# Optimization experiments

Hardware: AMD Instinct MI355X
Metric: run time of the kernel (lower is better)

Reference implementation:

```python
import jax, jax.numpy as jnp
import numpy as np

INFLUENCE_RADIUS = 8  # VectorizedTrajectoryComputer default


def compute_trajectories(emb):
    # emb: [B, S, D] -> [B, S, D]
    B, S, D = emb.shape
    diffs = emb[:, 1:] - emb[:, :-1]                      # [B, S-1, D]
    mag = jnp.linalg.norm(diffs, axis=-1, keepdims=True)  # [B, S-1, 1]
    ntraj = diffs / jnp.maximum(mag, 1e-8)                # normalized trajectories
    mw = jnp.tanh(mag[..., 0])                            # magnitude weights [B, S-1]
    pos = jnp.arange(S)[:, None]                          # [S, 1]
    j = jnp.arange(S - 1)[None, :]                        # [1, S-1]
    ws = jnp.maximum(0, pos - INFLUENCE_RADIUS)           # window start per pos
    mask = (j >= ws) & (j < pos)                          # window_end = pos (pos <= S-1)
    wsz = jnp.maximum(pos - ws, 1)                        # window size (>=1 to avoid /0)
    recency = jnp.where(mask, (j - ws + 1) / wsz, 0.0).astype(emb.dtype)  # [S, S-1]
    cw = mw[:, None, :] * recency[None]                   # combined weights [B, S, S-1]
    nw = cw / jnp.maximum(cw.sum(-1, keepdims=True), 1e-8)
    return jnp.einsum('bpj,bjd->bpd', nw, ntraj)          # [B, S, D]


def setup_inputs() -> dict:
    key = jax.random.key(0)
    ks = jax.random.split(key, 6)
    B, S, D = 2, 2048, 1024
    H, K, hd = 16, 16, 64
    return {
        'x': jax.random.normal(ks[0], (B, S, D), dtype=jnp.float32),
        'qkv_w': jax.random.normal(ks[1], (3 * D, D), dtype=jnp.float32) * 0.02,
        'out_w': jax.random.normal(ks[2], (D, D), dtype=jnp.float32) * 0.02,
        'splat_centers': jax.random.normal(ks[3], (H, K, hd), dtype=jnp.float32) * 0.02,
        'splat_log_scales': jnp.zeros((H, K), dtype=jnp.float32),
        'splat_amplitudes': jnp.ones((H, K), dtype=jnp.float32),
    }


def reference(x, qkv_w, out_w, splat_centers, splat_log_scales, splat_amplitudes):
    B, S, D = x.shape
    H, K, hd = splat_centers.shape
    # trajectories (computed when trajectories=None in forward)
    traj = compute_trajectories(x)
    # qkv projection (no bias)
    qkv = x @ qkv_w.T                                      # [B, S, 3D]
    q, k, v = jnp.split(qkv, 3, axis=-1)
    def heads(t):
        return t.reshape(B, S, H, hd).transpose(0, 2, 1, 3)  # [B, H, S, hd]
    q, k, v = heads(q), heads(k), heads(v)
    # squared distances to splat centers: [B, H, S, K]
    cn = jnp.sum(splat_centers ** 2, axis=-1)              # [H, K]
    def dists_sq(t):
        tn = jnp.sum(t ** 2, axis=-1, keepdims=True)       # [B, H, S, 1]
        cross = jnp.einsum('bhsd,hkd->bhsk', t, splat_centers)
        return tn - 2.0 * cross + cn[None, :, None, :]
    scales_sq = jnp.exp(splat_log_scales)[None, :, None, :] ** 2  # [1, H, 1, K]
    amp = jax.nn.sigmoid(splat_amplitudes)[None, :, None, :]
    q_weights = jnp.exp(-0.5 * dists_sq(q) / scales_sq) * amp     # [B, H, S, K]
    k_weights = jnp.exp(-0.5 * dists_sq(k) / scales_sq) * amp
    attn = jnp.einsum('bhis,bhjs->bhij', q_weights, k_weights)    # [B, H, S, S]
    attn = jax.nn.softmax(attn, axis=-1)
    out = jnp.einsum('bhij,bhjd->bhid', attn, v)                  # [B, H, S, hd]
    out = out.transpose(0, 2, 1, 3).reshape(B, S, D) @ out_w.T    # [B, S, D]
    return out, traj
```

## Files before the change

kernel.cpp:

```cpp
#include <hip/hip_runtime.h>
#include <math.h>

#define SEQ 2048
#define DIM 1024
#define NB  2
#define NH  16

typedef __attribute__((ext_vector_type(8))) short short8;
typedef __attribute__((ext_vector_type(4))) float floatx4;
typedef __attribute__((ext_vector_type(16))) float floatx16;

__device__ __forceinline__ ushort f2bf(float f) {
    unsigned u = __float_as_uint(f);
    return (ushort)((u + 0x7FFFu + ((u >> 16) & 1u)) >> 16);
}
__device__ __forceinline__ float bf2f(ushort h) {
    return __uint_as_float(((unsigned)h) << 16);
}
__device__ __forceinline__ void gload16(const void* g, char* lds_base) {
    __builtin_amdgcn_global_load_lds(
        (const __attribute__((address_space(1))) void*)g,
        (__attribute__((address_space(3))) void*)lds_base, 16, 0, 0);
}
__device__ __forceinline__ unsigned cvtpk(float a, float b) {
    unsigned r;
    asm("v_cvt_pk_bf16_f32 %0, %1, %2" : "=v"(r) : "v"(a), "v"(b));
    return r;
}
__device__ __forceinline__ void plswap(unsigned &a, unsigned &b) {
    asm("v_permlane32_swap_b32 %0, %1" : "+v"(a), "+v"(b));
}

__global__ __launch_bounds__(256) void front_kernel(
    const float* __restrict__ x, const float* __restrict__ qkv_w,
    ushort* __restrict__ xh, ushort* __restrict__ xl,
    ushort* __restrict__ wh, ushort* __restrict__ wlv,
    float* __restrict__ sbuf, float* __restrict__ invbuf)
{
    const int blk = blockIdx.x;
    if (blk < 4096) {
        int i = blk * 1024 + threadIdx.x * 4;
        float4 v = *(const float4*)(x + i);
        ushort4 h, l;
        h.x = f2bf(v.x); l.x = f2bf(v.x - bf2f(h.x));
        h.y = f2bf(v.y); l.y = f2bf(v.y - bf2f(h.y));
        h.z = f2bf(v.z); l.z = f2bf(v.z - bf2f(h.z));
        h.w = f2bf(v.w); l.w = f2bf(v.w - bf2f(h.w));
        *(ushort4*)(xh + i) = h;
        *(ushort4*)(xl + i) = l;
    } else if (blk < 6144) {
        int i = (blk - 4096) * 1024 + threadIdx.x * 4;
        float4 v = *(const float4*)(qkv_w + i);
        ushort4 o;
        o.x = f2bf(v.x); o.y = f2bf(v.y); o.z = f2bf(v.z); o.w = f2bf(v.w);
        *(ushort4*)(wh + i) = o;
    } else if (blk < 7168) {
        int i = (blk - 6144) * 1024 + threadIdx.x * 4;
        float4 v = *(const float4*)(qkv_w + 2097152 + i);
        ushort4 h, l;
        h.x = f2bf(v.x); l.x = f2bf(v.x - bf2f(h.x));
        h.y = f2bf(v.y); l.y = f2bf(v.y - bf2f(h.y));
        h.z = f2bf(v.z); l.z = f2bf(v.z - bf2f(h.z));
        h.w = f2bf(v.w); l.w = f2bf(v.w - bf2f(h.w));
        *(ushort4*)(wh + 2097152 + i) = h;
        *(ushort4*)(wlv + i) = l;
    } else {
        const int wave = threadIdx.x >> 6;
        const int lane = threadIdx.x & 63;
        const int row  = (blk - 7168) * 4 + wave;
        const int NR = NB * (SEQ - 1);
        if (row >= NR) return;
        const int b = row / (SEQ - 1);
        const int j = row - b * (SEQ - 1);
        const float* x0 = x + ((size_t)(b * SEQ + j)) * DIM;
        const float* x1 = x0 + DIM;
        float sum = 0.f;
        #pragma unroll
        for (int q = 0; q < 4; ++q) {
            int idx = q * 256 + lane * 4;
            float4 a = *(const float4*)(x0 + idx);
            float4 c = *(const float4*)(x1 + idx);
            float dx = c.x-a.x, dy = c.y-a.y, dz = c.z-a.z, dw = c.w-a.w;
            sum += dx*dx + dy*dy + dz*dz + dw*dw;
        }
        #pragma unroll
        for (int off = 32; off > 0; off >>= 1) sum += __shfl_down(sum, off);
        if (lane == 0) {
            float mag = sqrtf(sum);
            sbuf[row]   = tanhf(mag);
            invbuf[row] = 1.0f / fmaxf(mag, 1e-8f);
        }
    }
}

__device__ __forceinline__ void traj_body(
    int bp, const float* __restrict__ x, const float* __restrict__ sbuf,
    const float* __restrict__ invbuf, float* __restrict__ traj_out)
{
    const int b  = bp >> 11;
    const int p  = bp & (SEQ - 1);
    int ws = p - 8; if (ws < 0) ws = 0;
    const int wlen = p - ws;
    const float wsz = (float)((p - ws) > 1 ? (p - ws) : 1);
    const int base = b * (SEQ - 1) + ws;

    float Z = 0.f;
    for (int t = 0; t < wlen; ++t)
        Z += sbuf[base + t] * ((float)(t + 1) / wsz);
    const float scale = 1.0f / fmaxf(Z, 1e-8f);

    const int d0 = threadIdx.x * 4;
    const float* xb = x + ((size_t)(b * SEQ + ws)) * DIM + d0;
    float4 prev = *(const float4*)xb;
    float4 acc = make_float4(0.f,0.f,0.f,0.f);
    for (int t = 0; t < wlen; ++t) {
        xb += DIM;
        float4 cur = *(const float4*)xb;
        float cc = sbuf[base + t] * ((float)(t + 1) / wsz) * invbuf[base + t] * scale;
        acc.x += cc * (cur.x - prev.x);
        acc.y += cc * (cur.y - prev.y);
        acc.z += cc * (cur.z - prev.z);
        acc.w += cc * (cur.w - prev.w);
        prev = cur;
    }
    *(float4*)(traj_out + (size_t)bp * DIM + d0) = acc;
}

template<int SPLIT, int EPI, int BN>
__device__ __forceinline__ void gemm_body(
    int bx, int by, char* smem,
    const ushort* __restrict__ Ah, const ushort* __restrict__ Al,
    const ushort* __restrict__ Bh, const ushort* __restrict__ Bl,
    float* __restrict__ cout, int ldc,
    ushort* __restrict__ qwb, ushort* __restrict__ kwb)
{
    constexpr int JT   = BN / 32;
    constexpr int BSZ  = BN * 64;
    constexpr int HALF = 8192 + BSZ;
    const int tid = threadIdx.x;
    const int l = tid & 63;
    const int w = tid >> 6;
    const int wm = w >> 1, wn = w & 1;
    const int n0 = bx * BN;
    const int m0 = by * 128;

    char* a_h = smem;
    char* b_h = smem + 8192;
    char* a_l = smem + HALF;
    char* b_l = smem + HALF + 8192;

    const int srowA = 32 * w + (l >> 2);
    const int srowB = (BN == 128 ? 32 * w : 16 * w) + (l >> 2);
    const int scol  = (l & 3) * 8;
    const ushort* Ahg = Ah + (size_t)(m0 + srowA) * 1024 + scol;
    const ushort* Bhg = Bh + (size_t)(n0 + srowB) * 1024 + scol;
    const ushort* Alg = SPLIT ? Al + (size_t)(m0 + srowA) * 1024 + scol : nullptr;
    const ushort* Blg = SPLIT ? Bl + (size_t)(n0 + srowB) * 1024 + scol : nullptr;

    floatx4 acc[4][JT] = {};
    const int fr = l & 15;
    const int fq = (l >> 4) * 16;

    for (int kb = 0; kb < 1024; kb += 32) {
        if (kb) __syncthreads();
        gload16(Ahg + kb,             a_h + w*2048);
        gload16(Ahg + kb + 16*1024,   a_h + w*2048 + 1024);
        if (BN == 128) {
            gload16(Bhg + kb,             b_h + w*2048);
            gload16(Bhg + kb + 16*1024,   b_h + w*2048 + 1024);
        } else {
            gload16(Bhg + kb,             b_h + w*1024);
        }
        if (SPLIT) {
            gload16(Alg + kb,           a_l + w*2048);
            gload16(Alg + kb + 16*1024, a_l + w*2048 + 1024);
            if (BN == 128) {
                gload16(Blg + kb,           b_l + w*2048);
                gload16(Blg + kb + 16*1024, b_l + w*2048 + 1024);
            } else {
                gload16(Blg + kb,           b_l + w*1024);
            }
        }
        __syncthreads();
        short8 fah[4], fbh[JT], fal[4], fbl[JT];
        #pragma unroll
        for (int t = 0; t < 4; ++t) {
            fah[t] = *(const short8*)(a_h + ((wm*64 + t*16 + fr) << 6) + fq);
            if (SPLIT)
                fal[t] = *(const short8*)(a_l + ((wm*64 + t*16 + fr) << 6) + fq);
        }
        #pragma unroll
        for (int t = 0; t < JT; ++t) {
            fbh[t] = *(const short8*)(b_h + ((wn*(BN/2) + t*16 + fr) << 6) + fq);
            if (SPLIT)
                fbl[t] = *(const short8*)(b_l + ((wn*(BN/2) + t*16 + fr) << 6) + fq);
        }
        #pragma unroll
        for (int it = 0; it < 4; ++it)
            #pragma unroll
            for (int jt = 0; jt < JT; ++jt) {
                acc[it][jt] = __builtin_amdgcn_mfma_f32_16x16x32_bf16(
                    fah[it], fbh[jt], acc[it][jt], 0, 0, 0);
                if (SPLIT) {
                    acc[it][jt] = __builtin_amdgcn_mfma_f32_16x16x32_bf16(
                        fah[it], fbl[jt], acc[it][jt], 0, 0, 0);
                    acc[it][jt] = __builtin_amdgcn_mfma_f32_16x16x32_bf16(
                        fal[it], fbh[jt], acc[it][jt], 0, 0, 0);
                }
            }
    }

    const int row0 = (l >> 4) * 4;
    const int col  = l & 15;

    if (EPI == 0) {
        #pragma unroll
        for (int it = 0; it < 4; ++it)
            #pragma unroll
            for (int jt = 0; jt < JT; ++jt)
                #pragma unroll
                for (int r = 0; r < 4; ++r) {
                    int gm = m0 + wm*64 + it*16 + row0 + r;
                    int gn = n0 + wn*(BN/2) + jt*16 + col;
                    cout[(size_t)gm * ldc + gn] = acc[it][jt][r];
                }
    } else if (EPI == 2) {
        #pragma unroll
        for (int it = 0; it < 4; ++it)
            #pragma unroll
            for (int jt = 0; jt < JT; ++jt)
                #pragma unroll
                for (int r = 0; r < 4; ++r) {
                    int md = m0 + wm*64 + it*16 + row0 + r;
                    int t  = n0 + wn*(BN/2) + jt*16 + col;
                    int bb = t >> 11, ss = t & (SEQ - 1);
                    qwb[((size_t)bb << 21) + (size_t)md * SEQ + ss] = f2bf(acc[it][jt][r]);
                }
    } else {
        ushort* obuf = (n0 < 1024) ? qwb : kwb;
        const int nb = n0 & 1023;
        #pragma unroll
        for (int it = 0; it < 4; ++it)
            #pragma unroll
            for (int jt = 0; jt < JT; ++jt)
                #pragma unroll
                for (int r = 0; r < 4; ++r) {
                    int gm = m0 + wm*64 + it*16 + row0 + r;
                    int gn = nb + wn*(BN/2) + jt*16 + col;
                    int hh = gn >> 6, d = gn & 63;
                    int bb = gm >> 11, ss = gm & (SEQ - 1);
                    obuf[(((size_t)(bb*NH + hh))*SEQ + ss)*64 + d] = f2bf(acc[it][jt][r]);
                }
    }
}

__global__ __launch_bounds__(256) void gemmV_traj_kernel(
    const ushort* __restrict__ Ah, const ushort* __restrict__ Al,
    const ushort* __restrict__ Bh, const ushort* __restrict__ Bl,
    ushort* __restrict__ vbt,
    const float* __restrict__ x, const float* __restrict__ sbuf,
    const float* __restrict__ invbuf, float* __restrict__ traj_out)
{
    __shared__ __align__(16) char smem[2 * (8192 + 64*64)];
    const int blk = blockIdx.x;
    if (blk < 512) {
        gemm_body<1,2,64>(blk & 63, blk >> 6, smem, Ah, Al, Bh, Bl,
                          nullptr, 0, vbt, nullptr);
    } else {
        traj_body(blk - 512, x, sbuf, invbuf, traj_out);
    }
}

__global__ __launch_bounds__(256) void gemmQK_traj_kernel(
    const ushort* __restrict__ Ah, const ushort* __restrict__ Bh,
    ushort* __restrict__ qbuf, ushort* __restrict__ kbuf,
    const float* __restrict__ x, const float* __restrict__ sbuf,
    const float* __restrict__ invbuf, float* __restrict__ traj_out)
{
    __shared__ __align__(16) char smem[8192 + 128*64];
    const int blk = blockIdx.x;
    if (blk < 512) {
        gemm_body<0,3,128>(blk & 15, blk >> 4, smem, Ah, nullptr, Bh, nullptr,
                           nullptr, 0, qbuf, kbuf);
    } else {
        traj_body(blk - 512 + 2048, x, sbuf, invbuf, traj_out);
    }
}

__global__ __launch_bounds__(256) void gemmO_kernel(
    const ushort* __restrict__ Ah, const ushort* __restrict__ Al,
    const ushort* __restrict__ Bh, const ushort* __restrict__ Bl,
    float* __restrict__ cout)
{
    __shared__ __align__(16) char smem[2 * (8192 + 64*64)];
    gemm_body<1,0,64>(blockIdx.x, blockIdx.y, smem, Ah, Al, Bh, Bl,
                      cout, 1024, nullptr, nullptr);
}

__global__ __launch_bounds__(256) void splat_cvt_kernel(
    const ushort* __restrict__ qin, const ushort* __restrict__ kin,
    ushort* __restrict__ wq, ushort* __restrict__ wk,
    const float* __restrict__ centers, const float* __restrict__ lscales,
    const float* __restrict__ amps,
    const float* __restrict__ out_w, ushort* __restrict__ owh, ushort* __restrict__ owl)
{
    __shared__ float Cs[16*64];
    __shared__ float Pr[48];
    const int tid = threadIdx.x;
    if (blockIdx.x >= 512) {
        int i = (blockIdx.x - 512) * 1024 + tid * 4;
        float4 v = *(const float4*)(out_w + i);
        ushort4 h, l;
        h.x = f2bf(v.x); l.x = f2bf(v.x - bf2f(h.x));
        h.y = f2bf(v.y); l.y = f2bf(v.y - bf2f(h.y));
        h.z = f2bf(v.z); l.z = f2bf(v.z - bf2f(h.z));
        h.w = f2bf(v.w); l.w = f2bf(v.w - bf2f(h.w));
        *(ushort4*)(owh + i) = h;
        *(ushort4*)(owl + i) = l;
        return;
    }
    const int isK = blockIdx.x >> 8;
    const int bx  = blockIdx.x & 255;
    const ushort* qk = isK ? kin : qin;
    ushort* wout = isK ? wk : wq;
    const int bh  = bx >> 3;
    const int h   = bh & 15;
    const int s   = (bx & 7) * 256 + tid;
    {
        float4 c4 = *(const float4*)(centers + (size_t)h*1024 + tid*4);
        *(float4*)(Cs + tid*4) = c4;
    }
    if (tid < 16) {
        float s2 = __expf(2.f * lscales[h*16 + tid]);
        Pr[tid]      = -0.5f / s2;
        Pr[16 + tid] = 1.f / (1.f + __expf(-amps[h*16 + tid]));
        const float* cp = centers + ((size_t)h*16 + tid)*64;
        float cn = 0.f;
        for (int i = 0; i < 64; ++i) cn += cp[i]*cp[i];
        Pr[32 + tid] = cn;
    }
    __syncthreads();

    float q[64];
    const ushort* qp = qk + ((size_t)bh*SEQ + s)*64;
    #pragma unroll
    for (int i = 0; i < 8; ++i) {
        short8 v = *(const short8*)(qp + i*8);
        #pragma unroll
        for (int j = 0; j < 8; ++j) q[i*8+j] = bf2f((ushort)v[j]);
    }
    float tn = 0.f;
    #pragma unroll
    for (int i = 0; i < 64; ++i) tn = fmaf(q[i], q[i], tn);

    ushort o16[16];
    #pragma unroll 4
    for (int sp = 0; sp < 16; ++sp) {
        const float* cp = Cs + sp*64;
        float cr = 0.f;
        #pragma unroll
        for (int i = 0; i < 64; ++i) cr = fmaf(q[i], cp[i], cr);
        float dq = tn - 2.f*cr + Pr[32 + sp];
        o16[sp] = f2bf(__expf(dq * Pr[sp]) * Pr[16 + sp]);
    }
    ushort* op = wout + ((size_t)bh*SEQ + s)*16;
    *(short8*)(op)     = *(short8*)(o16);
    *(short8*)(op + 8) = *(short8*)(o16 + 8);
}

__global__ __launch_bounds__(256, 4) void attn_kernel(
    const ushort* __restrict__ qw, const ushort* __restrict__ kw,
    const ushort* __restrict__ vbt, ushort* __restrict__ hoh, ushort* __restrict__ hol)
{
    __shared__ __align__(16) char smem[16384 + 512];
    const int tid = threadIdx.x;
    const int l   = tid & 63;
    const int w   = tid >> 6;
    const int qh  = w >> 1;
    const int kh  = w & 1;
    const int l31 = l & 31;
    const int hi  = l >> 5;
    const int bh = blockIdx.y;
    const int b = bh >> 4;
    const int h = bh & 15;
    const int s0 = blockIdx.x * 64;

    short8 qf = *(const short8*)(qw + ((size_t)bh*SEQ + s0 + qh*32 + l31)*16 + hi*8);

    const ushort* kfp = kw + ((size_t)bh*SEQ + kh*32 + l31)*16 + hi*8;
    const ushort* vtb = vbt + ((size_t)(b*1024 + h*64))*SEQ;

    const int dA = w*16 + (l >> 3);
    const int dB = dA + 8;
    const ushort* vsA = vtb + (size_t)dA*SEQ + ((l & 7) ^ (dA & 7))*8;
    const ushort* vsB = vtb + (size_t)dB*SEQ + ((l & 7) ^ (dB & 7))*8;

    floatx16 acc0 = {}, acc1 = {};
    floatx16 zero16 = {};
    float zpart = 0.f;

    gload16(vsA, smem + w*2048);
    gload16(vsB, smem + w*2048 + 1024);
    short8 kf = *(const short8*)kfp;

    for (int jt = 0; jt < 32; ++jt) {
        __syncthreads();
        char* bufn = smem + ((jt + 1) & 1)*8192;
        if (jt < 31) {
            gload16(vsA + (jt + 1)*64, bufn + w*2048);
            gload16(vsB + (jt + 1)*64, bufn + w*2048 + 1024);
        }
        floatx16 sc = __builtin_amdgcn_mfma_f32_32x32x16_bf16(kf, qf, zero16, 0, 0, 0);
        if (jt < 31) kf = *(const short8*)(kfp + (jt + 1)*1024);

        float e[16];
        #pragma unroll
        for (int r = 0; r < 16; ++r) e[r] = __expf(sc[r]);
        float zs = 0.f;
        #pragma unroll
        for (int r = 0; r < 16; ++r) zs += e[r];
        zpart += zs;

        unsigned p0 = cvtpk(e[0],  e[1]),  p1 = cvtpk(e[2],  e[3]);
        unsigned p2 = cvtpk(e[4],  e[5]),  p3 = cvtpk(e[6],  e[7]);
        unsigned p4 = cvtpk(e[8],  e[9]),  p5 = cvtpk(e[10], e[11]);
        unsigned p6 = cvtpk(e[12], e[13]), p7 = cvtpk(e[14], e[15]);
        plswap(p0, p2); plswap(p1, p3);
        plswap(p4, p6); plswap(p5, p7);
        union { unsigned u[4]; short8 s; } ua, ub;
        ua.u[0] = p0; ua.u[1] = p1; ua.u[2] = p2; ua.u[3] = p3;
        ub.u[0] = p4; ub.u[1] = p5; ub.u[2] = p6; ub.u[3] = p7;

        const ushort* buf = (const ushort*)(smem + (jt & 1)*8192);
        #pragma unroll
        for (int dt = 0; dt < 2; ++dt) {
            int row = dt*32 + l31;
            const ushort* vr = buf + row*64;
            int bk0 = (kh*4 + hi)     ^ (row & 7);
            int bk1 = (kh*4 + 2 + hi) ^ (row & 7);
            short8 vb0 = *(const short8*)(vr + bk0*8);
            short8 vb1 = *(const short8*)(vr + bk1*8);
            if (dt == 0) {
                acc0 = __builtin_amdgcn_mfma_f32_32x32x16_bf16(ua.s, vb0, acc0, 0, 0, 0);
                acc0 = __builtin_amdgcn_mfma_f32_32x32x16_bf16(ub.s, vb1, acc0, 0, 0, 0);
            } else {
                acc1 = __builtin_amdgcn_mfma_f32_32x32x16_bf16(ua.s, vb0, acc1, 0, 0, 0);
                acc1 = __builtin_amdgcn_mfma_f32_32x32x16_bf16(ub.s, vb1, acc1, 0, 0, 0);
            }
        }
    }

    __syncthreads();

    float* cb = (float*)smem;
    float* zb = (float*)(smem + 16384);

    unsigned za = __float_as_uint(zpart), zc = za;
    plswap(za, zc);
    float zq = __uint_as_float(za) + __uint_as_float(zc);
    if (l31 == l) zb[kh*64 + qh*32 + l31] = zq;

    if (kh) {
        #pragma unroll
        for (int r = 0; r < 16; ++r) {
            int q = (r & 3) + 8*(r >> 2) + 4*hi;
            cb[(qh*32 + q)*64 + l31]      = acc0[r];
            cb[(qh*32 + q)*64 + 32 + l31] = acc1[r];
        }
    }
    __syncthreads();
    if (!kh) {
        #pragma unroll
        for (int r = 0; r < 16; ++r) {
            int q = (r & 3) + 8*(r >> 2) + 4*hi;
            float zt = zb[qh*32 + q] + zb[64 + qh*32 + q];
            float inv = 1.0f / zt;
            int s = s0 + qh*32 + q;
            size_t base = ((size_t)(b*SEQ + s))*1024 + h*64;
            float v0 = (acc0[r] + cb[(qh*32 + q)*64 + l31])      * inv;
            float v1 = (acc1[r] + cb[(qh*32 + q)*64 + 32 + l31]) * inv;
            ushort h0 = f2bf(v0);
            ushort h1 = f2bf(v1);
            hoh[base + l31]      = h0;
            hol[base + l31]      = f2bf(v0 - bf2f(h0));
            hoh[base + 32 + l31] = h1;
            hol[base + 32 + l31] = f2bf(v1 - bf2f(h1));
        }
    }
}

extern "C" void kernel_launch(void* const* d_in, const int* in_sizes, int n_in,
                              void* d_out, int out_size, void* d_ws, size_t ws_size,
                              hipStream_t stream)
{
    const float* x       = (const float*)d_in[0];
    const float* qkv_w   = (const float*)d_in[1];
    const float* out_w   = (const float*)d_in[2];
    const float* centers = (const float*)d_in[3];
    const float* lscales = (const float*)d_in[4];
    const float* amps    = (const float*)d_in[5];
    float* out  = (float*)d_out;
    float* traj = out + (size_t)NB*SEQ*DIM;

    char* wsb = (char*)d_ws;
    ushort* xh   = (ushort*)(wsb);
    ushort* xl   = (ushort*)(wsb + (8u<<20));
    ushort* wh   = (ushort*)(wsb + (16u<<20));
    ushort* wlv  = (ushort*)(wsb + (22u<<20));
    ushort* vbt  = (ushort*)(wsb + (24u<<20));
    float*  sbuf = (float*)(wsb + (40u<<20));
    float*  invb = sbuf + 4096;
    ushort* qbuf = xl;
    ushort* kbuf = (ushort*)(wsb + (32u<<20));
    ushort* qwbh = wlv;
    ushort* kwbh = wh + 2048*1024;
    ushort* owh  = wh;
    ushort* owl  = wh + 1048576;
    ushort* hoh  = xh;
    ushort* hol  = xl;

    front_kernel<<<8192, 256, 0, stream>>>(x, qkv_w, xh, xl, wh, wlv, sbuf, invb);
    gemmV_traj_kernel<<<2560, 256, 0, stream>>>(
        wh + 2048*1024, wlv, xh, xl, vbt, x, sbuf, invb, traj);
    gemmQK_traj_kernel<<<2560, 256, 0, stream>>>(
        xh, wh, qbuf, kbuf, x, sbuf, invb, traj);
    splat_cvt_kernel<<<1536, 256, 0, stream>>>(
        qbuf, kbuf, qwbh, kwbh, centers, lscales, amps, out_w, owh, owl);
    attn_kernel<<<dim3(32, 32), 256, 0, stream>>>(qwbh, kwbh, vbt, hoh, hol);
    gemmO_kernel<<<dim3(16, 32), 256, 0, stream>>>(hoh, hol, owh, owl, out);
}
```

Baseline: 245.8 us.

## Fuse splat weighting into QK GEMM epilogue and merge mid-stage kernels

The QK projection GEMM now computes Gaussian splat weights directly in its epilogue. It stages each wave's 64x64 tile through swizzled LDS and computes squared distances to the centers per token, so the bf16 Q/K intermediates are never written to global memory. The V GEMM, QK+splat GEMM and trajectory work are merged into one launch, and the out_w conversion moves into the front kernel. This cuts two launches and a global round-trip of Q/K, at the cost of a serial per-lane 16x64 distance loop in the epilogue and larger LDS use.

```diff
diff --git a/kernel.cpp b/kernel.cpp
--- a/kernel.cpp
+++ b/kernel.cpp
@@ -33,8 +33,10 @@
 
 __global__ __launch_bounds__(256) void front_kernel(
     const float* __restrict__ x, const float* __restrict__ qkv_w,
+    const float* __restrict__ out_w,
     ushort* __restrict__ xh, ushort* __restrict__ xl,
     ushort* __restrict__ wh, ushort* __restrict__ wlv,
+    ushort* __restrict__ owh, ushort* __restrict__ owl,
     float* __restrict__ sbuf, float* __restrict__ invbuf)
 {
     const int blk = blockIdx.x;
@@ -64,7 +66,7 @@
         h.w = f2bf(v.w); l.w = f2bf(v.w - bf2f(h.w));
         *(ushort4*)(wh + 2097152 + i) = h;
         *(ushort4*)(wlv + i) = l;
-    } else {
+    } else if (blk < 8192) {
         const int wave = threadIdx.x >> 6;
         const int lane = threadIdx.x & 63;
         const int row  = (blk - 7168) * 4 + wave;
@@ -90,6 +92,16 @@
             sbuf[row]   = tanhf(mag);
             invbuf[row] = 1.0f / fmaxf(mag, 1e-8f);
         }
+    } else {
+        int i = (blk - 8192) * 1024 + threadIdx.x * 4;
+        float4 v = *(const float4*)(out_w + i);
+        ushort4 h, l;
+        h.x = f2bf(v.x); l.x = f2bf(v.x - bf2f(h.x));
+        h.y = f2bf(v.y); l.y = f2bf(v.y - bf2f(h.y));
+        h.z = f2bf(v.z); l.z = f2bf(v.z - bf2f(h.z));
+        h.w = f2bf(v.w); l.w = f2bf(v.w - bf2f(h.w));
+        *(ushort4*)(owh + i) = h;
+        *(ushort4*)(owl + i) = l;
     }
 }
 
@@ -132,7 +144,7 @@
     const ushort* __restrict__ Ah, const ushort* __restrict__ Al,
     const ushort* __restrict__ Bh, const ushort* __restrict__ Bl,
     float* __restrict__ cout, int ldc,
-    ushort* __restrict__ qwb, ushort* __restrict__ kwb)
+    ushort* __restrict__ qwb)
 {
     constexpr int JT   = BN / 32;
     constexpr int BSZ  = BN * 64;
@@ -224,7 +236,7 @@
                     int gn = n0 + wn*(BN/2) + jt*16 + col;
                     cout[(size_t)gm * ldc + gn] = acc[it][jt][r];
                 }
-    } else if (EPI == 2) {
+    } else {
         #pragma unroll
         for (int it = 0; it < 4; ++it)
             #pragma unroll
@@ -236,54 +248,134 @@
                     int bb = t >> 11, ss = t & (SEQ - 1);
                     qwb[((size_t)bb << 21) + (size_t)md * SEQ + ss] = f2bf(acc[it][jt][r]);
                 }
-    } else {
-        ushort* obuf = (n0 < 1024) ? qwb : kwb;
-        const int nb = n0 & 1023;
+    }
+}
+
+__device__ __forceinline__ void qk_splat_body(
+    int bx, int by, char* smem,
+    const ushort* __restrict__ Ah, const ushort* __restrict__ Bh,
+    ushort* __restrict__ qwb, ushort* __restrict__ kwb,
+    const float* __restrict__ centers, const float* __restrict__ lscales,
+    const float* __restrict__ amps)
+{
+    const int tid = threadIdx.x;
+    const int l = tid & 63;
+    const int w = tid >> 6;
+    const int wm = w >> 1, wn = w & 1;
+    const int n0 = bx * 128;
+    const int m0 = by * 128;
+    char* a_h = smem;
+    char* b_h = smem + 8192;
+    float* Cst = (float*)(smem + 32768);
+
+    {
+        const float* src = centers + (size_t)((n0 & 1023) >> 6) * 1024;
+        float4 v0 = *(const float4*)(src + tid*8);
+        float4 v1 = *(const float4*)(src + tid*8 + 4);
+        *(float4*)(Cst + tid*8)     = v0;
+        *(float4*)(Cst + tid*8 + 4) = v1;
+    }
+
+    const int srow = 32 * w + (l >> 2);
+    const int scol = (l & 3) * 8;
+    const ushort* Ahg = Ah + (size_t)(m0 + srow) * 1024 + scol;
+    const ushort* Bhg = Bh + (size_t)(n0 + srow) * 1024 + scol;
+
+    floatx4 acc[4][4] = {};
+    const int fr = l & 15;
+    const int fq = (l >> 4) * 16;
+
+    for (int kb = 0; kb < 1024; kb += 32) {
+        if (kb) __syncthreads();
+        gload16(Ahg + kb,             a_h + w*2048);
+        gload16(Ahg + kb + 16*1024,   a_h + w*2048 + 1024);
+        gload16(Bhg + kb,             b_h + w*2048);
+        gload16(Bhg + kb + 16*1024,   b_h + w*2048 + 1024);
+        __syncthreads();
+        short8 fah[4], fbh[4];
+        #pragma unroll
+        for (int t = 0; t < 4; ++t) {
+            fah[t] = *(const short8*)(a_h + ((wm*64 + t*16 + fr) << 6) + fq);
+            fbh[t] = *(const short8*)(b_h + ((wn*64 + t*16 + fr) << 6) + fq);
+        }
         #pragma unroll
         for (int it = 0; it < 4; ++it)
             #pragma unroll
-            for (int jt = 0; jt < JT; ++jt)
-                #pragma unroll
-                for (int r = 0; r < 4; ++r) {
-                    int gm = m0 + wm*64 + it*16 + row0 + r;
-                    int gn = nb + wn*(BN/2) + jt*16 + col;
-                    int hh = gn >> 6, d = gn & 63;
-                    int bb = gm >> 11, ss = gm & (SEQ - 1);
-                    obuf[(((size_t)(bb*NH + hh))*SEQ + ss)*64 + d] = f2bf(acc[it][jt][r]);
-                }
-    }
-}
-
-__global__ __launch_bounds__(256) void gemmV_traj_kernel(
-    const ushort* __restrict__ Ah, const ushort* __restrict__ Al,
-    const ushort* __restrict__ Bh, const ushort* __restrict__ Bl,
-    ushort* __restrict__ vbt,
+            for (int jt = 0; jt < 4; ++jt)
+                acc[it][jt] = __builtin_amdgcn_mfma_f32_16x16x32_bf16(
+                    fah[it], fbh[jt], acc[it][jt], 0, 0, 0);
+    }
+
+    __syncthreads();
+    const int row0 = (l >> 4) * 4;
+    const int col  = l & 15;
+    ushort* qt = (ushort*)(smem + w*8192);
+
+    #pragma unroll
+    for (int it = 0; it < 4; ++it)
+        #pragma unroll
+        for (int jt = 0; jt < 4; ++jt)
+            #pragma unroll
+            for (int r = 0; r < 4; ++r) {
+                int tok = it*16 + row0 + r;
+                int c   = jt*16 + col;
+                qt[tok*64 + ((((c >> 3) ^ (tok & 7)) << 3) | (c & 7))] =
+                    f2bf(acc[it][jt][r]);
+            }
+
+    float qv[64];
+    #pragma unroll
+    for (int j = 0; j < 8; ++j) {
+        short8 v = *(const short8*)(qt + l*64 + ((j ^ (l & 7)) << 3));
+        #pragma unroll
+        for (int i = 0; i < 8; ++i) qv[j*8 + i] = bf2f((ushort)v[i]);
+    }
+
+    const int hh = ((n0 & 1023) + wn*64) >> 6;
+    const float* cw = Cst + wn*1024;
+    const int tg = m0 + wm*64 + l;
+    const int bb = tg >> 11, ss = tg & (SEQ - 1);
+    ushort* obuf = (n0 < 1024) ? qwb : kwb;
+
+    ushort o16[16];
+    #pragma unroll
+    for (int sp = 0; sp < 16; ++sp) {
+        const float* cp = cw + sp*64;
+        float dq = 0.f;
+        #pragma unroll
+        for (int i = 0; i < 64; ++i) {
+            float t = qv[i] - cp[i];
+            dq = fmaf(t, t, dq);
+        }
+        float s2 = __expf(2.f * lscales[hh*16 + sp]);
+        float pa = 1.f / (1.f + __expf(-amps[hh*16 + sp]));
+        o16[sp] = f2bf(__expf(dq * (-0.5f / s2)) * pa);
+    }
+    ushort* op = obuf + (((size_t)(bb*NH + hh))*SEQ + ss)*16;
+    *(short8*)(op)     = *(short8*)(o16);
+    *(short8*)(op + 8) = *(short8*)(o16 + 8);
+}
+
+__global__ __launch_bounds__(256) void mid_kernel(
+    const ushort* __restrict__ xh, const ushort* __restrict__ xl,
+    const ushort* __restrict__ wh, const ushort* __restrict__ wlv,
+    ushort* __restrict__ vbt, ushort* __restrict__ qwb, ushort* __restrict__ kwb,
+    const float* __restrict__ centers, const float* __restrict__ lscales,
+    const float* __restrict__ amps,
     const float* __restrict__ x, const float* __restrict__ sbuf,
-    const float* __restrict__ invbuf, float* __restrict__ traj_out)
-{
-    __shared__ __align__(16) char smem[2 * (8192 + 64*64)];
+    const float* __restrict__ invb, float* __restrict__ traj_out)
+{
+    __shared__ __align__(16) char smem[40960];
     const int blk = blockIdx.x;
     if (blk < 512) {
-        gemm_body<1,2,64>(blk & 63, blk >> 6, smem, Ah, Al, Bh, Bl,
-                          nullptr, 0, vbt, nullptr);
+        gemm_body<1,2,64>(blk & 63, blk >> 6, smem,
+                          wh + 2048*1024, wlv, xh, xl, nullptr, 0, vbt);
+    } else if (blk < 1024) {
+        const int g = blk - 512;
+        qk_splat_body(g & 15, g >> 4, smem, xh, wh,
+                      qwb, kwb, centers, lscales, amps);
     } else {
-        traj_body(blk - 512, x, sbuf, invbuf, traj_out);
-    }
-}
-
-__global__ __launch_bounds__(256) void gemmQK_traj_kernel(
-    const ushort* __restrict__ Ah, const ushort* __restrict__ Bh,
-    ushort* __restrict__ qbuf, ushort* __restrict__ kbuf,
-    const float* __restrict__ x, const float* __restrict__ sbuf,
-    const float* __restrict__ invbuf, float* __restrict__ traj_out)
-{
-    __shared__ __align__(16) char smem[8192 + 128*64];
-    const int blk = blockIdx.x;
-    if (blk < 512) {
-        gemm_body<0,3,128>(blk & 15, blk >> 4, smem, Ah, nullptr, Bh, nullptr,
-                           nullptr, 0, qbuf, kbuf);
-    } else {
-        traj_body(blk - 512 + 2048, x, sbuf, invbuf, traj_out);
+        traj_body(blk - 1024, x, sbuf, invb, traj_out);
     }
 }
 
@@ -294,78 +386,7 @@
 {
     __shared__ __align__(16) char smem[2 * (8192 + 64*64)];
     gemm_body<1,0,64>(blockIdx.x, blockIdx.y, smem, Ah, Al, Bh, Bl,
-                      cout, 1024, nullptr, nullptr);
-}
-
-__global__ __launch_bounds__(256) void splat_cvt_kernel(
-    const ushort* __restrict__ qin, const ushort* __restrict__ kin,
-    ushort* __restrict__ wq, ushort* __restrict__ wk,
-    const float* __restrict__ centers, const float* __restrict__ lscales,
-    const float* __restrict__ amps,
-    const float* __restrict__ out_w, ushort* __restrict__ owh, ushort* __restrict__ owl)
-{
-    __shared__ float Cs[16*64];
-    __shared__ float Pr[48];
-    const int tid = threadIdx.x;
-    if (blockIdx.x >= 512) {
-        int i = (blockIdx.x - 512) * 1024 + tid * 4;
-        float4 v = *(const float4*)(out_w + i);
-        ushort4 h, l;
-        h.x = f2bf(v.x); l.x = f2bf(v.x - bf2f(h.x));
-        h.y = f2bf(v.y); l.y = f2bf(v.y - bf2f(h.y));
-        h.z = f2bf(v.z); l.z = f2bf(v.z - bf2f(h.z));
-        h.w = f2bf(v.w); l.w = f2bf(v.w - bf2f(h.w));
-        *(ushort4*)(owh + i) = h;
-        *(ushort4*)(owl + i) = l;
-        return;
-    }
-    const int isK = blockIdx.x >> 8;
-    const int bx  = blockIdx.x & 255;
-    const ushort* qk = isK ? kin : qin;
-    ushort* wout = isK ? wk : wq;
-    const int bh  = bx >> 3;
-    const int h   = bh & 15;
-    const int s   = (bx & 7) * 256 + tid;
-    {
-        float4 c4 = *(const float4*)(centers + (size_t)h*1024 + tid*4);
-        *(float4*)(Cs + tid*4) = c4;
-    }
-    if (tid < 16) {
-        float s2 = __expf(2.f * lscales[h*16 + tid]);
-        Pr[tid]      = -0.5f / s2;
-        Pr[16 + tid] = 1.f / (1.f + __expf(-amps[h*16 + tid]));
-        const float* cp = centers + ((size_t)h*16 + tid)*64;
-        float cn = 0.f;
-        for (int i = 0; i < 64; ++i) cn += cp[i]*cp[i];
-        Pr[32 + tid] = cn;
-    }
-    __syncthreads();
-
-    float q[64];
-    const ushort* qp = qk + ((size_t)bh*SEQ + s)*64;
-    #pragma unroll
-    for (int i = 0; i < 8; ++i) {
-        short8 v = *(const short8*)(qp + i*8);
-        #pragma unroll
-        for (int j = 0; j < 8; ++j) q[i*8+j] = bf2f((ushort)v[j]);
-    }
-    float tn = 0.f;
-    #pragma unroll
-    for (int i = 0; i < 64; ++i) tn = fmaf(q[i], q[i], tn);
-
-    ushort o16[16];
-    #pragma unroll 4
-    for (int sp = 0; sp < 16; ++sp) {
-        const float* cp = Cs + sp*64;
-        float cr = 0.f;
-        #pragma unroll
-        for (int i = 0; i < 64; ++i) cr = fmaf(q[i], cp[i], cr);
-        float dq = tn - 2.f*cr + Pr[32 + sp];
-        o16[sp] = f2bf(__expf(dq * Pr[sp]) * Pr[16 + sp]);
-    }
-    ushort* op = wout + ((size_t)bh*SEQ + s)*16;
-    *(short8*)(op)     = *(short8*)(o16);
-    *(short8*)(op + 8) = *(short8*)(o16 + 8);
+                      cout, 1024, nullptr);
 }
 
 __global__ __launch_bounds__(256, 4) void attn_kernel(
@@ -508,24 +529,20 @@
     ushort* wh   = (ushort*)(wsb + (16u<<20));
     ushort* wlv  = (ushort*)(wsb + (22u<<20));
     ushort* vbt  = (ushort*)(wsb + (24u<<20));
+    ushort* owh  = (ushort*)(wsb + (32u<<20));
+    ushort* owl  = (ushort*)(wsb + (34u<<20));
+    ushort* qwbh = (ushort*)(wsb + (36u<<20));
+    ushort* kwbh = (ushort*)(wsb + (38u<<20));
     float*  sbuf = (float*)(wsb + (40u<<20));
     float*  invb = sbuf + 4096;
-    ushort* qbuf = xl;
-    ushort* kbuf = (ushort*)(wsb + (32u<<20));
-    ushort* qwbh = wlv;
-    ushort* kwbh = wh + 2048*1024;
-    ushort* owh  = wh;
-    ushort* owl  = wh + 1048576;
     ushort* hoh  = xh;
     ushort* hol  = xl;
 
-    front_kernel<<<8192, 256, 0, stream>>>(x, qkv_w, xh, xl, wh, wlv, sbuf, invb);
-    gemmV_traj_kernel<<<2560, 256, 0, stream>>>(
-        wh + 2048*1024, wlv, xh, xl, vbt, x, sbuf, invb, traj);
-    gemmQK_traj_kernel<<<2560, 256, 0, stream>>>(
-        xh, wh, qbuf, kbuf, x, sbuf, invb, traj);
-    splat_cvt_kernel<<<1536, 256, 0, stream>>>(
-        qbuf, kbuf, qwbh, kwbh, centers, lscales, amps, out_w, owh, owl);
+    front_kernel<<<9216, 256, 0, stream>>>(
+        x, qkv_w, out_w, xh, xl, wh, wlv, owh, owl, sbuf, invb);
+    mid_kernel<<<5120, 256, 0, stream>>>(
+        xh, xl, wh, wlv, vbt, qwbh, kwbh, centers, lscales, amps,
+        x, sbuf, invb, traj);
     attn_kernel<<<dim3(32, 32), 256, 0, stream>>>(qwbh, kwbh, vbt, hoh, hol);
     gemmO_kernel<<<dim3(16, 32), 256, 0, stream>>>(hoh, hol, owh, owl, out);
 }
```

Result: slower. 255.9 us (+4.1%).
